# Kernel optimization log

Measured on AMD Instinct MI355X. Metric: run time of the kernel, lower is better.

Reference implementation:

```python
import jax, jax.numpy as jnp
import numpy as np

D_MODEL = 1024
N_HEADS = 16
D_HEAD = D_MODEL // N_HEADS


def setup_inputs() -> dict:
    key = jax.random.key(0)
    ks = jax.random.split(key, 9)
    s = 1.0 / np.sqrt(D_MODEL)
    x = jax.random.normal(ks[0], (2, 2048, D_MODEL), dtype=jnp.float32)
    # torch nn.Linear stores weight [out, in]; we store [in, out] for x @ W
    Wq = jax.random.uniform(ks[1], (D_MODEL, D_MODEL), jnp.float32, -s, s)
    bq = jax.random.uniform(ks[2], (D_MODEL,), jnp.float32, -s, s)
    Wk = jax.random.uniform(ks[3], (D_MODEL, D_MODEL), jnp.float32, -s, s)
    bk = jax.random.uniform(ks[4], (D_MODEL,), jnp.float32, -s, s)
    Wv = jax.random.uniform(ks[5], (D_MODEL, D_MODEL), jnp.float32, -s, s)
    bv = jax.random.uniform(ks[6], (D_MODEL,), jnp.float32, -s, s)
    Wo = jax.random.uniform(ks[7], (D_MODEL, D_MODEL), jnp.float32, -s, s)
    bo = jax.random.uniform(ks[8], (D_MODEL,), jnp.float32, -s, s)
    return {"x": x, "Wq": Wq, "bq": bq, "Wk": Wk, "bk": bk,
            "Wv": Wv, "bv": bv, "Wo": Wo, "bo": bo}


def reference(x, Wq, bq, Wk, bk, Wv, bv, Wo, bo):
    B, S, _ = x.shape
    # project and split heads: [B, H, S, Dh]
    def split(t):
        return t.reshape(B, S, N_HEADS, D_HEAD).transpose(0, 2, 1, 3)
    Q = split(x @ Wq + bq)
    K = split(x @ Wk + bk)
    V = split(x @ Wv + bv)
    scale = 1.0 / jnp.sqrt(jnp.asarray(D_HEAD, x.dtype))
    scores = jnp.einsum('bhqd,bhkd->bhqk', Q, K) * scale  # [B,H,S,S]
    attn = jax.nn.softmax(scores, axis=-1)
    out = jnp.einsum('bhqk,bhkd->bhqd', attn, V)  # [B,H,S,Dh]
    out = out.transpose(0, 2, 1, 3).reshape(B, S, D_MODEL)
    return out @ Wo + bo
```

## Files before the change

### kernel.cpp

```cpp
#include <hip/hip_runtime.h>
#include <hip/hip_bf16.h>
#include <cmath>

#define D_MODEL 1024
#define N_HEADS 16
#define D_HEAD  64
#define BATCH   2
#define SEQ     2048
#define M_TOT   (BATCH*SEQ)
#define NELT    ((size_t)M_TOT * D_MODEL)

typedef __attribute__((ext_vector_type(8)))  short short8;
typedef __attribute__((ext_vector_type(4)))  float f32x4;
typedef __attribute__((ext_vector_type(16))) float f32x16;
typedef __attribute__((ext_vector_type(4)))  unsigned uint4v;

#define QSCALE (0.125f * 1.44269504088896f)

static __device__ __forceinline__ ushort f2bf(float f) {
    __hip_bfloat16 h = __float2bfloat16(f);
    return *reinterpret_cast<ushort*>(&h);
}

static __device__ __forceinline__ unsigned cvtpk_bf16(float lo, float hi) {
    unsigned r;
    asm("v_cvt_pk_bf16_f32 %0, %1, %2" : "=v"(r) : "v"(lo), "v"(hi));
    return r;
}

static __device__ __forceinline__ void gload_lds16(const void* g, void* l) {
    __builtin_amdgcn_global_load_lds((const __attribute__((address_space(1))) unsigned*)g,
                                     (__attribute__((address_space(3))) unsigned*)l,
                                     16, 0, 0);
}

__global__ __launch_bounds__(256)
void f32_to_bf16_kernel(const float* __restrict__ in, ushort* __restrict__ out, int n4)
{
    const int i = blockIdx.x * 256 + threadIdx.x;
    if (i < n4) {
        const float4 v = ((const float4*)in)[i];
        ushort4 u;
        u.x = f2bf(v.x); u.y = f2bf(v.y); u.z = f2bf(v.z); u.w = f2bf(v.w);
        ((ushort4*)out)[i] = u;
    }
}

__global__ __launch_bounds__(256)
void transpose_w4_kernel(const float* __restrict__ W0, const float* __restrict__ W1,
                         const float* __restrict__ W2, const float* __restrict__ W3,
                         ushort* __restrict__ Wt0)
{
    __shared__ float Ts[64][65];
    const int z = blockIdx.z;
    const float* W = (z == 0) ? W0 : (z == 1) ? W1 : (z == 2) ? W2 : W3;
    ushort* Wt = Wt0 + (size_t)z * D_MODEL * D_MODEL;

    const int t  = threadIdx.x;
    const int n0 = blockIdx.x * 64;
    const int k0 = blockIdx.y * 64;
    const int rr = t >> 4;
    const int c4 = (t & 15) * 4;

#pragma unroll
    for (int i = 0; i < 4; ++i) {
        const int r = rr + i * 16;
        const float4 v = *(const float4*)&W[(size_t)(k0 + r) * D_MODEL + n0 + c4];
        Ts[r][c4 + 0] = v.x; Ts[r][c4 + 1] = v.y;
        Ts[r][c4 + 2] = v.z; Ts[r][c4 + 3] = v.w;
    }
    __syncthreads();
#pragma unroll
    for (int i = 0; i < 4; ++i) {
        const int nn = rr + i * 16;
        ushort4 u;
        u.x = f2bf(Ts[c4 + 0][nn]); u.y = f2bf(Ts[c4 + 1][nn]);
        u.z = f2bf(Ts[c4 + 2][nn]); u.w = f2bf(Ts[c4 + 3][nn]);
        *(ushort4*)&Wt[(size_t)(n0 + nn) * D_MODEL + k0 + c4] = u;
    }
}

__global__ __launch_bounds__(256)
void gemm_qkv_mfma(const ushort* __restrict__ A, const ushort* __restrict__ Bt,
                   const float* __restrict__ bq, const float* __restrict__ bk,
                   const float* __restrict__ bv, ushort* __restrict__ QKV)
{
    __shared__ ushort As[128 * 64];
    __shared__ ushort Bs[128 * 64];

    const int t    = threadIdx.x;
    const int lane = t & 63;
    const int w    = t >> 6;
    const int wr   = w >> 1;
    const int wc   = w & 1;
    const int l16  = lane & 15;
    const int g    = lane >> 4;
    const int m0   = blockIdx.y * 128;
    const int n0   = blockIdx.x * 128;

    f32x4 acc[4][4];
#pragma unroll
    for (int i = 0; i < 4; ++i)
#pragma unroll
        for (int j = 0; j < 4; ++j) acc[i][j] = f32x4{0.f, 0.f, 0.f, 0.f};

    for (int kt = 0; kt < D_MODEL; kt += 64) {
        __syncthreads();
        const ushort* Ag = A  + (size_t)m0 * D_MODEL + kt;
        const ushort* Bg = Bt + (size_t)n0 * D_MODEL + kt;
#pragma unroll
        for (int it = 0; it < 4; ++it) {
            const int b   = (it * 256 + t) * 16;
            const int row = b >> 7;
            const int src = (b & 127) ^ ((row & 7) << 4);
            const int lof = (it * 256 + (t & ~63)) * 8;
            gload_lds16(Ag + (size_t)row * D_MODEL + (src >> 1), As + lof);
            gload_lds16(Bg + (size_t)row * D_MODEL + (src >> 1), Bs + lof);
        }
        __syncthreads();

#pragma unroll
        for (int kh = 0; kh < 2; ++kh) {
            short8 a[4], bfr[4];
#pragma unroll
            for (int fm = 0; fm < 4; ++fm) {
                const int row  = wr * 64 + fm * 16 + l16;
                const int byte = row * 128 + (((kh << 6) | (g << 4)) ^ ((row & 7) << 4));
                a[fm] = *(const short8*)((const char*)As + byte);
            }
#pragma unroll
            for (int fn = 0; fn < 4; ++fn) {
                const int row  = wc * 64 + fn * 16 + l16;
                const int byte = row * 128 + (((kh << 6) | (g << 4)) ^ ((row & 7) << 4));
                bfr[fn] = *(const short8*)((const char*)Bs + byte);
            }
#pragma unroll
            for (int fm = 0; fm < 4; ++fm)
#pragma unroll
                for (int fn = 0; fn < 4; ++fn)
                    acc[fm][fn] = __builtin_amdgcn_mfma_f32_16x16x32_bf16(a[fm], bfr[fn], acc[fm][fn], 0, 0, 0);
        }
    }

#pragma unroll
    for (int fm = 0; fm < 4; ++fm) {
        const int mb  = m0 + wr * 64 + fm * 16 + g * 4;
        const int bb  = mb >> 11;
        const int sA  = mb & (SEQ - 1);
#pragma unroll
        for (int fn = 0; fn < 4; ++fn) {
            const int n    = n0 + wc * 64 + fn * 16 + l16;
            const int proj = n >> 10;
            const int nn   = n & 1023;
            const int h    = nn >> 6;
            const int dh   = nn & 63;
            const float bn = (proj == 0) ? bq[nn] : (proj == 1) ? bk[nn] : bv[nn];
            if (proj == 2) {
                ushort4 pk;
                pk.x = f2bf(acc[fm][fn][0] + bn);
                pk.y = f2bf(acc[fm][fn][1] + bn);
                pk.z = f2bf(acc[fm][fn][2] + bn);
                pk.w = f2bf(acc[fm][fn][3] + bn);
                *(ushort4*)&QKV[2 * NELT +
                                (((size_t)(bb * N_HEADS + h)) * D_HEAD + dh) * SEQ + sA] = pk;
            } else {
                const float sc = (proj == 0) ? QSCALE : 1.0f;
                ushort* outp = QKV + (size_t)proj * NELT;
#pragma unroll
                for (int r = 0; r < 4; ++r) {
                    const float c = (acc[fm][fn][r] + bn) * sc;
                    outp[(((size_t)(bb * N_HEADS + h)) * SEQ + sA + r) * D_HEAD + dh] = f2bf(c);
                }
            }
        }
    }
}

__global__ __launch_bounds__(256)
void gemm_out_mfma(const ushort* __restrict__ A, const ushort* __restrict__ Bt,
                   const float* __restrict__ bias, float* __restrict__ outp)
{
    __shared__ ushort As[128 * 64];
    __shared__ ushort Bs[128 * 64];

    const int t    = threadIdx.x;
    const int lane = t & 63;
    const int w    = t >> 6;
    const int wr   = w >> 1;
    const int wc   = w & 1;
    const int l16  = lane & 15;
    const int g    = lane >> 4;
    const int m0   = blockIdx.y * 128;
    const int n0   = blockIdx.x * 128;

    f32x4 acc[4][4];
#pragma unroll
    for (int i = 0; i < 4; ++i)
#pragma unroll
        for (int j = 0; j < 4; ++j) acc[i][j] = f32x4{0.f, 0.f, 0.f, 0.f};

    for (int kt = 0; kt < D_MODEL; kt += 64) {
        __syncthreads();
        const ushort* Ag = A  + (size_t)m0 * D_MODEL + kt;
        const ushort* Bg = Bt + (size_t)n0 * D_MODEL + kt;
#pragma unroll
        for (int it = 0; it < 4; ++it) {
            const int b   = (it * 256 + t) * 16;
            const int row = b >> 7;
            const int src = (b & 127) ^ ((row & 7) << 4);
            const int lof = (it * 256 + (t & ~63)) * 8;
            gload_lds16(Ag + (size_t)row * D_MODEL + (src >> 1), As + lof);
            gload_lds16(Bg + (size_t)row * D_MODEL + (src >> 1), Bs + lof);
        }
        __syncthreads();

#pragma unroll
        for (int kh = 0; kh < 2; ++kh) {
            short8 a[4], bfr[4];
#pragma unroll
            for (int fm = 0; fm < 4; ++fm) {
                const int row  = wr * 64 + fm * 16 + l16;
                const int byte = row * 128 + (((kh << 6) | (g << 4)) ^ ((row & 7) << 4));
                a[fm] = *(const short8*)((const char*)As + byte);
            }
#pragma unroll
            for (int fn = 0; fn < 4; ++fn) {
                const int row  = wc * 64 + fn * 16 + l16;
                const int byte = row * 128 + (((kh << 6) | (g << 4)) ^ ((row & 7) << 4));
                bfr[fn] = *(const short8*)((const char*)Bs + byte);
            }
#pragma unroll
            for (int fm = 0; fm < 4; ++fm)
#pragma unroll
                for (int fn = 0; fn < 4; ++fn)
                    acc[fm][fn] = __builtin_amdgcn_mfma_f32_16x16x32_bf16(a[fm], bfr[fn], acc[fm][fn], 0, 0, 0);
        }
    }

#pragma unroll
    for (int fm = 0; fm < 4; ++fm) {
        const int mb = m0 + wr * 64 + fm * 16 + g * 4;
#pragma unroll
        for (int fn = 0; fn < 4; ++fn) {
            const int n  = n0 + wc * 64 + fn * 16 + l16;
            const float bn = bias[n];
#pragma unroll
            for (int r = 0; r < 4; ++r)
                outp[(size_t)(mb + r) * D_MODEL + n] = acc[fm][fn][r] + bn;
        }
    }
}

__global__ __launch_bounds__(256)
void flash_attn_mfma32(const ushort* __restrict__ Q, const ushort* __restrict__ K,
                       const ushort* __restrict__ Vt, ushort* __restrict__ AO)
{
    __shared__ ushort Kl[2][64 * 64];
    __shared__ ushort Vl[2][64 * 64];
    __shared__ float  Alds[4][32];

    const int t    = threadIdx.x;
    const int w    = t >> 6;
    const int lane = t & 63;
    const int l32  = lane & 31;
    const int h    = lane >> 5;
    const int qt   = blockIdx.x;
    const int bh   = blockIdx.y;

    const int q0 = qt * 128 + w * 32;
    const size_t qkbase = (size_t)bh * SEQ * D_HEAD;
    const ushort* Vg0 = Vt + (size_t)bh * D_HEAD * SEQ;

    short8 qf[4];
    {
        const ushort* qp = Q + qkbase + (size_t)(q0 + l32) * D_HEAD + h * 8;
#pragma unroll
        for (int ks = 0; ks < 4; ++ks)
            qf[ks] = *(const short8*)(qp + ks * 16);
    }

    f32x16 o[2];
#pragma unroll
    for (int dt = 0; dt < 2; ++dt)
#pragma unroll
        for (int r = 0; r < 16; ++r) o[dt][r] = 0.f;
    float m_r = -INFINITY, l_r = 0.f;

    auto stage = [&](int ktile, int b) {
        const ushort* Kg = K + qkbase + (size_t)(ktile * 64) * D_HEAD;
        const ushort* Vg = Vg0 + ktile * 64;
#pragma unroll
        for (int it = 0; it < 2; ++it) {
            const int bb  = (it * 256 + t) * 16;
            const int row = bb >> 7;
            const int src = (bb & 127) ^ ((row & 7) << 4);
            const int lof = (it * 256 + (t & ~63)) * 8;
            gload_lds16(Kg + (size_t)row * D_HEAD + (src >> 1), &Kl[b][lof]);
            gload_lds16(Vg + (size_t)row * SEQ + (src >> 1), &Vl[b][lof]);
        }
    };

    stage(0, 0);
    __syncthreads();

    const int NT = SEQ / 64;
    for (int kt = 0; kt < NT; ++kt) {
        const int buf = kt & 1;
        if (kt + 1 < NT) stage(kt + 1, buf ^ 1);

        short8 kf[2][4];
#pragma unroll
        for (int nt = 0; nt < 2; ++nt) {
            const int row = nt * 32 + l32;
#pragma unroll
            for (int ks = 0; ks < 4; ++ks) {
                const int byte = row * 128 + ((ks * 32 + h * 16) ^ ((row & 7) << 4));
                kf[nt][ks] = *(const short8*)((const char*)&Kl[buf][0] + byte);
            }
        }
        short8 vf[2][4];
#pragma unroll
        for (int dt = 0; dt < 2; ++dt) {
            const int row = dt * 32 + l32;
#pragma unroll
            for (int ks = 0; ks < 4; ++ks) {
                const int byte = row * 128 + ((ks * 32 + h * 16) ^ ((row & 7) << 4));
                vf[dt][ks] = *(const short8*)((const char*)&Vl[buf][0] + byte);
            }
        }

        f32x16 st[2];
#pragma unroll
        for (int nt = 0; nt < 2; ++nt)
#pragma unroll
            for (int r = 0; r < 16; ++r) st[nt][r] = 0.f;
        __builtin_amdgcn_s_setprio(1);
#pragma unroll
        for (int ks = 0; ks < 4; ++ks) {
            st[0] = __builtin_amdgcn_mfma_f32_32x32x16_bf16(kf[0][ks], qf[ks], st[0], 0, 0, 0);
            st[1] = __builtin_amdgcn_mfma_f32_32x32x16_bf16(kf[1][ks], qf[ks], st[1], 0, 0, 0);
        }
        __builtin_amdgcn_s_setprio(0);

        float pmax = st[0][0];
#pragma unroll
        for (int r = 1; r < 16; ++r) pmax = fmaxf(pmax, st[0][r]);
#pragma unroll
        for (int r = 0; r < 16; ++r) pmax = fmaxf(pmax, st[1][r]);
        pmax = fmaxf(pmax, __shfl_xor(pmax, 32, 64));

        if (__any(pmax - m_r > 8.f)) {
            const float mnew  = fmaxf(m_r, pmax);
            const float alpha = exp2f(m_r - mnew);
            m_r = mnew;
            l_r *= alpha;
            Alds[w][l32] = alpha;
            float4 av[4];
#pragma unroll
            for (int a = 0; a < 4; ++a)
                av[a] = *(const float4*)&Alds[w][8 * a + 4 * h];
#pragma unroll
            for (int dt = 0; dt < 2; ++dt)
#pragma unroll
                for (int r = 0; r < 16; ++r)
                    o[dt][r] *= ((const float*)&av[r >> 2])[r & 3];
        }

        float rs = 0.f;
        unsigned c[2][4][2];
#pragma unroll
        for (int nt = 0; nt < 2; ++nt) {
            float p[16];
#pragma unroll
            for (int r = 0; r < 16; ++r) {
                p[r] = exp2f(st[nt][r] - m_r);
                rs += p[r];
            }
#pragma unroll
            for (int a = 0; a < 4; ++a) {
                c[nt][a][0] = cvtpk_bf16(p[4 * a + 0], p[4 * a + 1]);
                c[nt][a][1] = cvtpk_bf16(p[4 * a + 2], p[4 * a + 3]);
            }
        }
        rs += __shfl_xor(rs, 32, 64);
        l_r += rs;

        short8 pa[4];
#pragma unroll
        for (int nt = 0; nt < 2; ++nt) {
#pragma unroll
            for (int half = 0; half < 2; ++half) {
                auto s0 = __builtin_amdgcn_permlane32_swap(c[nt][2 * half + 0][0],
                                                           c[nt][2 * half + 1][0], false, false);
                auto s1 = __builtin_amdgcn_permlane32_swap(c[nt][2 * half + 0][1],
                                                           c[nt][2 * half + 1][1], false, false);
                uint4v u;
                u[0] = s0[0]; u[1] = s1[0]; u[2] = s0[1]; u[3] = s1[1];
                pa[nt * 2 + half] = __builtin_bit_cast(short8, u);
            }
        }

        __builtin_amdgcn_s_setprio(1);
#pragma unroll
        for (int ks = 0; ks < 4; ++ks) {
            o[0] = __builtin_amdgcn_mfma_f32_32x32x16_bf16(pa[ks], vf[0][ks], o[0], 0, 0, 0);
            o[1] = __builtin_amdgcn_mfma_f32_32x32x16_bf16(pa[ks], vf[1][ks], o[1], 0, 0, 0);
        }
        __builtin_amdgcn_s_setprio(0);

        __syncthreads();
    }

    Alds[w][l32] = l_r;
    float4 lv[4];
#pragma unroll
    for (int a = 0; a < 4; ++a)
        lv[a] = *(const float4*)&Alds[w][8 * a + 4 * h];

    const int b  = bh >> 4;
    const int hh = bh & 15;
#pragma unroll
    for (int r = 0; r < 16; ++r) {
        const int qrow = (r & 3) + 8 * (r >> 2) + 4 * h;
        const float inv = 1.f / ((const float*)&lv[r >> 2])[r & 3];
        const size_t row = (size_t)b * SEQ + q0 + qrow;
#pragma unroll
        for (int dt = 0; dt < 2; ++dt)
            AO[row * D_MODEL + hh * D_HEAD + dt * 32 + l32] = f2bf(o[dt][r] * inv);
    }
}

extern "C" void kernel_launch(void* const* d_in, const int* in_sizes, int n_in,
                              void* d_out, int out_size, void* d_ws, size_t ws_size,
                              hipStream_t stream)
{
    const float* x  = (const float*)d_in[0];
    const float* Wq = (const float*)d_in[1];
    const float* bq = (const float*)d_in[2];
    const float* Wk = (const float*)d_in[3];
    const float* bk = (const float*)d_in[4];
    const float* Wv = (const float*)d_in[5];
    const float* bv = (const float*)d_in[6];
    const float* Wo = (const float*)d_in[7];
    const float* bo = (const float*)d_in[8];
    float* out = (float*)d_out;

    const size_t WELT = (size_t)D_MODEL * D_MODEL;
    ushort* xb  = (ushort*)d_ws;
    ushort* Wqt = xb + NELT;
    ushort* Wot = Wqt + 3 * WELT;
    ushort* Qb  = xb + 2 * NELT;
    ushort* Kb  = Qb + NELT;
    ushort* Vtb = Kb + NELT;
    ushort* AOb = xb + 5 * NELT;

    f32_to_bf16_kernel<<<dim3(M_TOT * D_MODEL / 4 / 256), 256, 0, stream>>>(x, xb, M_TOT * D_MODEL / 4);
    transpose_w4_kernel<<<dim3(D_MODEL / 64, D_MODEL / 64, 4), 256, 0, stream>>>(Wq, Wk, Wv, Wo, Wqt);
    gemm_qkv_mfma<<<dim3(3 * D_MODEL / 128, M_TOT / 128), 256, 0, stream>>>(xb, Wqt, bq, bk, bv, Qb);
    flash_attn_mfma32<<<dim3(SEQ / 128, BATCH * N_HEADS), 256, 0, stream>>>(Qb, Kb, Vtb, AOb);
    gemm_out_mfma<<<dim3(D_MODEL / 128, M_TOT / 128), 256, 0, stream>>>(AOb, Wot, bo, out);
}
```

Measured before the change: 153.1 us.

## Split attention KV range in two and merge partial outputs in separate kernel

Attention blocks now each process half of the key/value sequence, doubling the grid so more blocks run concurrently per CU. Each half writes a normalized bf16 partial output plus per-row max and sum, and a new merge kernel combines them with log-sum-exp weights into the head-interleaved layout. The row max and row sum reductions are rewritten as trees to shorten dependency chains. This adds an extra kernel launch and extra global traffic for the partial outputs, plus an extra bf16 rounding step.

```diff
diff --git a/kernel.cpp b/kernel.cpp
--- a/kernel.cpp
+++ b/kernel.cpp
@@ -20,6 +20,9 @@
 static __device__ __forceinline__ ushort f2bf(float f) {
     __hip_bfloat16 h = __float2bfloat16(f);
     return *reinterpret_cast<ushort*>(&h);
+}
+static __device__ __forceinline__ float bf2f(short u) {
+    return __uint_as_float(((unsigned)(ushort)u) << 16);
 }
 
 static __device__ __forceinline__ unsigned cvtpk_bf16(float lo, float hi) {
@@ -252,8 +255,9 @@
 }
 
 __global__ __launch_bounds__(256)
-void flash_attn_mfma32(const ushort* __restrict__ Q, const ushort* __restrict__ K,
-                       const ushort* __restrict__ Vt, ushort* __restrict__ AO)
+void flash_attn_split32(const ushort* __restrict__ Q, const ushort* __restrict__ K,
+                        const ushort* __restrict__ Vt, ushort* __restrict__ Opart,
+                        float2* __restrict__ ML)
 {
     __shared__ ushort Kl[2][64 * 64];
     __shared__ ushort Vl[2][64 * 64];
@@ -264,7 +268,8 @@
     const int lane = t & 63;
     const int l32  = lane & 31;
     const int h    = lane >> 5;
-    const int qt   = blockIdx.x;
+    const int hv   = blockIdx.x & 1;
+    const int qt   = blockIdx.x >> 1;
     const int bh   = blockIdx.y;
 
     const int q0 = qt * 128 + w * 32;
@@ -300,13 +305,13 @@
         }
     };
 
-    stage(0, 0);
+    const int it0 = hv * 16;
+    stage(it0, 0);
     __syncthreads();
 
-    const int NT = SEQ / 64;
-    for (int kt = 0; kt < NT; ++kt) {
+    for (int kt = 0; kt < 16; ++kt) {
         const int buf = kt & 1;
-        if (kt + 1 < NT) stage(kt + 1, buf ^ 1);
+        if (kt + 1 < 16) stage(it0 + kt + 1, buf ^ 1);
 
         short8 kf[2][4];
 #pragma unroll
@@ -342,12 +347,15 @@
         }
         __builtin_amdgcn_s_setprio(0);
 
-        float pmax = st[0][0];
-#pragma unroll
-        for (int r = 1; r < 16; ++r) pmax = fmaxf(pmax, st[0][r]);
-#pragma unroll
-        for (int r = 0; r < 16; ++r) pmax = fmaxf(pmax, st[1][r]);
-        pmax = fmaxf(pmax, __shfl_xor(pmax, 32, 64));
+        float mx[8];
+#pragma unroll
+        for (int r = 0; r < 8; ++r)
+            mx[r] = fmaxf(fmaxf(st[0][r], st[0][r + 8]), fmaxf(st[1][r], st[1][r + 8]));
+#pragma unroll
+        for (int s = 4; s > 0; s >>= 1)
+#pragma unroll
+            for (int r = 0; r < s; ++r) mx[r] = fmaxf(mx[r], mx[r + s]);
+        const float pmax = fmaxf(mx[0], __shfl_xor(mx[0], 32, 64));
 
         if (__any(pmax - m_r > 8.f)) {
             const float mnew  = fmaxf(m_r, pmax);
@@ -366,21 +374,29 @@
                     o[dt][r] *= ((const float*)&av[r >> 2])[r & 3];
         }
 
-        float rs = 0.f;
+        float rs;
         unsigned c[2][4][2];
-#pragma unroll
-        for (int nt = 0; nt < 2; ++nt) {
-            float p[16];
-#pragma unroll
-            for (int r = 0; r < 16; ++r) {
-                p[r] = exp2f(st[nt][r] - m_r);
-                rs += p[r];
-            }
-#pragma unroll
-            for (int a = 0; a < 4; ++a) {
-                c[nt][a][0] = cvtpk_bf16(p[4 * a + 0], p[4 * a + 1]);
-                c[nt][a][1] = cvtpk_bf16(p[4 * a + 2], p[4 * a + 3]);
-            }
+        {
+            float part[2];
+#pragma unroll
+            for (int nt = 0; nt < 2; ++nt) {
+                float pv[16];
+#pragma unroll
+                for (int r = 0; r < 16; ++r) pv[r] = exp2f(st[nt][r] - m_r);
+#pragma unroll
+                for (int a = 0; a < 4; ++a) {
+                    c[nt][a][0] = cvtpk_bf16(pv[4 * a + 0], pv[4 * a + 1]);
+                    c[nt][a][1] = cvtpk_bf16(pv[4 * a + 2], pv[4 * a + 3]);
+                }
+                float s8[8];
+#pragma unroll
+                for (int r = 0; r < 8; ++r) s8[r] = pv[2 * r] + pv[2 * r + 1];
+                float s4[4];
+#pragma unroll
+                for (int r = 0; r < 4; ++r) s4[r] = s8[2 * r] + s8[2 * r + 1];
+                part[nt] = (s4[0] + s4[1]) + (s4[2] + s4[3]);
+            }
+            rs = part[0] + part[1];
         }
         rs += __shfl_xor(rs, 32, 64);
         l_r += rs;
@@ -411,23 +427,58 @@
         __syncthreads();
     }
 
+    if (h == 0)
+        ML[(size_t)hv * BATCH * N_HEADS * SEQ + (size_t)bh * SEQ + q0 + l32] =
+            make_float2(m_r, l_r);
+
     Alds[w][l32] = l_r;
     float4 lv[4];
 #pragma unroll
     for (int a = 0; a < 4; ++a)
         lv[a] = *(const float4*)&Alds[w][8 * a + 4 * h];
 
-    const int b  = bh >> 4;
-    const int hh = bh & 15;
 #pragma unroll
     for (int r = 0; r < 16; ++r) {
         const int qrow = (r & 3) + 8 * (r >> 2) + 4 * h;
         const float inv = 1.f / ((const float*)&lv[r >> 2])[r & 3];
-        const size_t row = (size_t)b * SEQ + q0 + qrow;
+        const size_t row = (size_t)bh * SEQ + q0 + qrow;
 #pragma unroll
         for (int dt = 0; dt < 2; ++dt)
-            AO[row * D_MODEL + hh * D_HEAD + dt * 32 + l32] = f2bf(o[dt][r] * inv);
-    }
+            Opart[(size_t)hv * NELT + row * D_HEAD + dt * 32 + l32] =
+                f2bf(o[dt][r] * inv);
+    }
+}
+
+__global__ __launch_bounds__(256)
+void merge_attn(const ushort* __restrict__ Opart, const float2* __restrict__ ML,
+                ushort* __restrict__ AO)
+{
+    const int idx = blockIdx.x * 256 + threadIdx.x;
+    const int dh8 = idx & 7;
+    const int s   = (idx >> 3) & (SEQ - 1);
+    const int bh  = idx >> 14;
+    const size_t rowh = (size_t)bh * SEQ + s;
+
+    const float2 ml1 = ML[rowh];
+    const float2 ml2 = ML[(size_t)BATCH * N_HEADS * SEQ + rowh];
+    const float m   = fmaxf(ml1.x, ml2.x);
+    const float c1  = ml1.y * exp2f(ml1.x - m);
+    const float c2  = ml2.y * exp2f(ml2.x - m);
+    const float inv = 1.f / (c1 + c2);
+    const float w1  = c1 * inv;
+    const float w2  = c2 * inv;
+
+    const size_t off = rowh * D_HEAD + dh8 * 8;
+    const short8 o1 = *(const short8*)&Opart[off];
+    const short8 o2 = *(const short8*)&Opart[NELT + off];
+    short8 res;
+#pragma unroll
+    for (int j = 0; j < 8; ++j)
+        res[j] = (short)f2bf(w1 * bf2f(o1[j]) + w2 * bf2f(o2[j]));
+
+    const int b = bh >> 4;
+    const int h = bh & 15;
+    *(short8*)&AO[((size_t)b * SEQ + s) * D_MODEL + h * D_HEAD + dh8 * 8] = res;
 }
 
 extern "C" void kernel_launch(void* const* d_in, const int* in_sizes, int n_in,
@@ -446,17 +497,20 @@
     float* out = (float*)d_out;
 
     const size_t WELT = (size_t)D_MODEL * D_MODEL;
-    ushort* xb  = (ushort*)d_ws;
-    ushort* Wqt = xb + NELT;
-    ushort* Wot = Wqt + 3 * WELT;
-    ushort* Qb  = xb + 2 * NELT;
-    ushort* Kb  = Qb + NELT;
-    ushort* Vtb = Kb + NELT;
-    ushort* AOb = xb + 5 * NELT;
+    ushort* xb    = (ushort*)d_ws;
+    ushort* Wqt   = xb + NELT;
+    ushort* Wot   = Wqt + 3 * WELT;
+    ushort* Qb    = xb + 2 * NELT;
+    ushort* Kb    = Qb + NELT;
+    ushort* Vtb   = Kb + NELT;
+    ushort* Opart = xb + 5 * NELT;
+    float2* ML    = (float2*)(xb + 7 * NELT);
+    ushort* AOb   = xb;
 
     f32_to_bf16_kernel<<<dim3(M_TOT * D_MODEL / 4 / 256), 256, 0, stream>>>(x, xb, M_TOT * D_MODEL / 4);
     transpose_w4_kernel<<<dim3(D_MODEL / 64, D_MODEL / 64, 4), 256, 0, stream>>>(Wq, Wk, Wv, Wo, Wqt);
     gemm_qkv_mfma<<<dim3(3 * D_MODEL / 128, M_TOT / 128), 256, 0, stream>>>(xb, Wqt, bq, bk, bv, Qb);
-    flash_attn_mfma32<<<dim3(SEQ / 128, BATCH * N_HEADS), 256, 0, stream>>>(Qb, Kb, Vtb, AOb);
+    flash_attn_split32<<<dim3(2 * SEQ / 128, BATCH * N_HEADS), 256, 0, stream>>>(Qb, Kb, Vtb, Opart, ML);
+    merge_attn<<<dim3(BATCH * N_HEADS * SEQ * 8 / 256), 256, 0, stream>>>(Opart, ML, AOb);
     gemm_out_mfma<<<dim3(D_MODEL / 128, M_TOT / 128), 256, 0, stream>>>(AOb, Wot, bo, out);
 }
```

Result: slower. 164.8 us (+7.7%).
